# Kernel tuning notes

Measured on AMD Instinct MI355X. Metric: run time of the kernel, lower is better.

The kernel has to match this reference:

```python
import jax, jax.numpy as jnp
import numpy as np

N_INP = 1024
N_HID = 1024
N_OUT = 1024
B, S = 8, 2048


def setup_inputs() -> dict:
    key = jax.random.key(0)
    ks = jax.random.split(key, 9)
    s_in = 1.0 / np.sqrt(N_INP)
    s_hid = 1.0 / np.sqrt(N_HID)
    return {
        "x": jax.random.normal(ks[0], (B, S, N_INP), jnp.float32),
        "wq": jax.random.uniform(ks[1], (N_INP, N_HID), jnp.float32, -s_in, s_in),
        "bq": jax.random.uniform(ks[2], (N_HID,), jnp.float32, -s_in, s_in),
        "wk": jax.random.uniform(ks[3], (N_INP, N_HID), jnp.float32, -s_in, s_in),
        "bk": jax.random.uniform(ks[4], (N_HID,), jnp.float32, -s_in, s_in),
        "wv": jax.random.uniform(ks[5], (N_INP, N_HID), jnp.float32, -s_in, s_in),
        "bv": jax.random.uniform(ks[6], (N_HID,), jnp.float32, -s_in, s_in),
        "wo": jax.random.uniform(ks[7], (N_HID, N_OUT), jnp.float32, -s_hid, s_hid),
        "bo": jax.random.uniform(ks[8], (N_OUT,), jnp.float32, -s_hid, s_hid),
    }


def reference(x, wq, bq, wk, bk, wv, bv, wo, bo):
    # x: [B, S, n_inp]
    q = jnp.einsum("bsi,ih->bsh", x, wq) + bq  # [B,S,H]
    k = jnp.einsum("bsi,ih->bsh", x, wk) + bk
    v = jnp.einsum("bsi,ih->bsh", x, wv) + bv
    scale = 1.0 / jnp.sqrt(jnp.float32(N_HID))
    energy = jnp.einsum("bqh,bkh->bqk", q, k) * scale  # [B,S,S]
    attn = jax.nn.softmax(energy, axis=-1)  # dropout=0.0 (eval)
    ctx = jnp.einsum("bqk,bkh->bqh", attn, v)  # [B,S,H]
    out = jnp.einsum("bsh,ho->bso", ctx, wo) + bo  # [B,S,n_out]
    return out
```

## Files before the change

kernel.cpp:

```cpp
#include <hip/hip_runtime.h>
#include <hip/hip_bf16.h>


typedef __attribute__((ext_vector_type(8))) __bf16 bf16x8;
typedef __attribute__((ext_vector_type(4))) __bf16 bf16x4;
typedef __attribute__((ext_vector_type(4))) float  f32x4;
typedef __attribute__((ext_vector_type(8))) float  f32x8;

__device__ __forceinline__ void gl_lds16(const void* g, void* l) {
    __builtin_amdgcn_global_load_lds(
        (__attribute__((address_space(1))) const void*)g,
        (__attribute__((address_space(3))) void*)l, 16, 0, 0);
}

__global__ __launch_bounds__(256) void k_convert(const float* __restrict__ in,
                                                 __bf16* __restrict__ out) {
    const int i = blockIdx.x * 256 + threadIdx.x;
    f32x8 a = *((const f32x8*)in + i);
    bf16x8 o;
#pragma unroll
    for (int j = 0; j < 8; ++j) o[j] = (__bf16)a[j];
    *((bf16x8*)out + i) = o;
}

__global__ __launch_bounds__(256) void k_transpose_w(
    const float* __restrict__ w0, const float* __restrict__ w1,
    const float* __restrict__ w2, const float* __restrict__ w3,
    __bf16* __restrict__ Wt) {
    const int z = blockIdx.z;
    const float* W = (z == 0) ? w0 : (z == 1) ? w1 : (z == 2) ? w2 : w3;
    __bf16* Wo = Wt + (long long)z * 1048576;
    __shared__ float t[64][65];
    const int tid = threadIdx.x;
    const int c4 = (tid & 15) * 4, r0 = tid >> 4;
    const int bx = blockIdx.x * 64, by = blockIdx.y * 64;
#pragma unroll
    for (int p = 0; p < 4; ++p) {
        const int r = r0 + p * 16;
        f32x4 v = *(const f32x4*)(W + (long long)(by + r) * 1024 + bx + c4);
#pragma unroll
        for (int j = 0; j < 4; ++j) t[r][c4 + j] = v[j];
    }
    __syncthreads();
#pragma unroll
    for (int p = 0; p < 4; ++p) {
        const int r = r0 + p * 16;
        bf16x4 o;
#pragma unroll
        for (int j = 0; j < 4; ++j) o[j] = (__bf16)t[c4 + j][r];
        *(bf16x4*)(Wo + (long long)(bx + r) * 1024 + by + c4) = o;
    }
}

__global__ __launch_bounds__(256) void k_bcat(const float* __restrict__ bq,
                                              const float* __restrict__ bk,
                                              const float* __restrict__ bv,
                                              float* __restrict__ bc) {
    const int i = blockIdx.x * 256 + threadIdx.x;
    const float* s = (i < 1024) ? bq : (i < 2048 ? bk : bv);
    bc[i] = s[i & 1023];
}

__global__ __launch_bounds__(256) void k_softmax(__bf16* __restrict__ E) {
    __bf16* p = E + (long long)blockIdx.x * 2048;
    const int tid = threadIdx.x, l = tid & 63, w = tid >> 6;
    bf16x8 vb = *((const bf16x8*)p + tid);
    float v[8];
#pragma unroll
    for (int i = 0; i < 8; ++i) v[i] = (float)vb[i];
    float m = v[0];
#pragma unroll
    for (int i = 1; i < 8; ++i) m = fmaxf(m, v[i]);
    for (int off = 32; off > 0; off >>= 1) m = fmaxf(m, __shfl_xor(m, off));
    __shared__ float redm[4], reds[4];
    if (l == 0) redm[w] = m;
    __syncthreads();
    m = fmaxf(fmaxf(redm[0], redm[1]), fmaxf(redm[2], redm[3]));
    float e[8], s = 0.f;
#pragma unroll
    for (int i = 0; i < 8; ++i) { e[i] = __expf(v[i] - m); s += e[i]; }
    for (int off = 32; off > 0; off >>= 1) s += __shfl_xor(s, off);
    if (l == 0) reds[w] = s;
    __syncthreads();
    s = reds[0] + reds[1] + reds[2] + reds[3];
    const float inv = 1.0f / s;
    bf16x8 o;
#pragma unroll
    for (int i = 0; i < 8; ++i) o[i] = (__bf16)(e[i] * inv);
    *((bf16x8*)p + tid) = o;
}

template <int MODE, bool HAS_BIAS>
__global__ __launch_bounds__(512, 2) void gemm_bt(
    const __bf16* __restrict__ A, const __bf16* __restrict__ Bt,
    const float* __restrict__ bias, void* __restrict__ Cout,
    int K, int lda, int ldb, int ldc, int gy, int rpx, int bnc,
    float scale, long long sA, long long sB, long long sC) {
    __shared__ __align__(16) __bf16 Abuf0[16384];
    __shared__ __align__(16) __bf16 Bbuf0[16384];
    __shared__ __align__(16) __bf16 Abuf1[16384];
    __shared__ __align__(16) __bf16 Bbuf1[16384];

    const int lid = blockIdx.x;
    const int xcd = lid & 7;
    const int jj = lid >> 3;
    const int bn = jj % bnc;
    const int rt = xcd * rpx + jj / bnc;
    const int z = rt / gy;
    const int bm = rt - z * gy;

    const __bf16* Ab = A + (long long)z * sA;
    const __bf16* Bb = Bt + (long long)z * sB;

    const int tid = threadIdx.x;
    const int l = tid & 63, w = tid >> 6;
    const int wm = w >> 2, wn = w & 3;

    const int rA = tid >> 3;
    const int cswz = (tid & 7) ^ (rA & 3);
    const __bf16* aSg = Ab + (long long)(bm * 256 + rA) * lda + cswz * 8;
    const __bf16* bSg = Bb + (long long)(bn * 256 + rA) * ldb + cswz * 8;
    const long long a64 = (long long)lda * 64;
    const long long b64 = (long long)ldb * 64;
    const int ldst = tid * 16;

    const int r16 = l & 15, kq4 = l >> 4;
    const int swz = kq4 ^ (r16 & 3);
    const int aro = (wm * 128 + r16) * 64 + swz * 8;
    const int bro = (wn * 64 + r16) * 64 + swz * 8;

    f32x4 acc[8][4] = {};
    bf16x8 bf[4][2];

#define ST_A(buf, j, t)                                                    \
    gl_lds16(aSg + (j) * a64 + (long long)(t) * 64,                        \
             (char*)(buf) + ldst + (j) * 8192)
#define ST_B(buf, j, t)                                                    \
    gl_lds16(bSg + (j) * b64 + (long long)(t) * 64,                        \
             (char*)(buf) + ldst + (j) * 8192)

#define RD_B(buf)                                                          \
    do {                                                                   \
        _Pragma("unroll") for (int ni = 0; ni < 4; ++ni) {                 \
            bf[ni][0] = *(const bf16x8*)((buf) + bro + ni * 1024);         \
            bf[ni][1] = *(const bf16x8*)((buf) + bro + ni * 1024 + 32);    \
        }                                                                  \
    } while (0)

#define WV4 asm volatile("s_waitcnt vmcnt(4)" ::: "memory")
#define WV0 asm volatile("s_waitcnt vmcnt(0)" ::: "memory")
#define NOW ((void)0)

#define PHASE(Abuf, p, RB, RBUF, STAGES, WAIT)                                 \
    do {                                                                      \
        bf16x8 af0k0 = *(const bf16x8*)((Abuf) + aro + (2 * (p)) * 1024);      \
        bf16x8 af0k1 = *(const bf16x8*)((Abuf) + aro + (2 * (p)) * 1024 + 32); \
        bf16x8 af1k0 = *(const bf16x8*)((Abuf) + aro + (2 * (p) + 1) * 1024);  \
        bf16x8 af1k1 = *(const bf16x8*)((Abuf) + aro + (2*(p)+1) * 1024 + 32); \
        if (RB) RD_B(RBUF);                                                   \
        STAGES;                                                               \
        __builtin_amdgcn_s_barrier();                                         \
        asm volatile("s_waitcnt lgkmcnt(0)" ::: "memory");                    \
        __builtin_amdgcn_sched_barrier(0);                                    \
        __builtin_amdgcn_s_setprio(1);                                        \
        _Pragma("unroll") for (int ni = 0; ni < 4; ++ni) {                    \
            acc[2 * (p)][ni] = __builtin_amdgcn_mfma_f32_16x16x32_bf16(       \
                af0k0, bf[ni][0], acc[2 * (p)][ni], 0, 0, 0);                 \
            acc[2 * (p)][ni] = __builtin_amdgcn_mfma_f32_16x16x32_bf16(       \
                af0k1, bf[ni][1], acc[2 * (p)][ni], 0, 0, 0);                 \
            acc[2 * (p) + 1][ni] = __builtin_amdgcn_mfma_f32_16x16x32_bf16(   \
                af1k0, bf[ni][0], acc[2 * (p) + 1][ni], 0, 0, 0);             \
            acc[2 * (p) + 1][ni] = __builtin_amdgcn_mfma_f32_16x16x32_bf16(   \
                af1k1, bf[ni][1], acc[2 * (p) + 1][ni], 0, 0, 0);             \
        }                                                                     \
        __builtin_amdgcn_s_setprio(0);                                        \
        WAIT;                                                                 \
        __builtin_amdgcn_sched_barrier(0);                                    \
        __builtin_amdgcn_s_barrier();                                         \
    } while (0)

    ST_B(Bbuf0, 0, 0); ST_B(Bbuf0, 1, 0); ST_B(Bbuf0, 2, 0); ST_B(Bbuf0, 3, 0);
    ST_A(Abuf0, 0, 0); ST_A(Abuf0, 1, 0); ST_A(Abuf0, 2, 0); ST_A(Abuf0, 3, 0);
    ST_B(Bbuf1, 0, 1); ST_B(Bbuf1, 1, 1); ST_B(Bbuf1, 2, 1); ST_B(Bbuf1, 3, 1);
    WV4;
    __builtin_amdgcn_s_barrier();

    const int NT = K >> 6;
    for (int t0 = 0; t0 + 3 < NT; t0 += 2) {
        PHASE(Abuf0, 0, 1, Bbuf0,
              (ST_A(Abuf1, 0, t0 + 1), ST_A(Abuf1, 1, t0 + 1),
               ST_A(Abuf1, 2, t0 + 1), ST_A(Abuf1, 3, t0 + 1)), NOW);
        PHASE(Abuf0, 1, 0, Bbuf0,
              (ST_B(Bbuf0, 0, t0 + 2), ST_B(Bbuf0, 1, t0 + 2)), NOW);
        PHASE(Abuf0, 2, 0, Bbuf0,
              (ST_B(Bbuf0, 2, t0 + 2), ST_B(Bbuf0, 3, t0 + 2)), NOW);
        PHASE(Abuf0, 3, 0, Bbuf0, NOW, WV4);
        PHASE(Abuf1, 0, 1, Bbuf1,
              (ST_A(Abuf0, 0, t0 + 2), ST_A(Abuf0, 1, t0 + 2)), NOW);
        PHASE(Abuf1, 1, 0, Bbuf1,
              (ST_A(Abuf0, 2, t0 + 2), ST_A(Abuf0, 3, t0 + 2)), NOW);
        PHASE(Abuf1, 2, 0, Bbuf1,
              (ST_B(Bbuf1, 0, t0 + 3), ST_B(Bbuf1, 1, t0 + 3)), NOW);
        PHASE(Abuf1, 3, 0, Bbuf1,
              (ST_B(Bbuf1, 2, t0 + 3), ST_B(Bbuf1, 3, t0 + 3)), WV4);
    }
    {
        PHASE(Abuf0, 0, 1, Bbuf0,
              (ST_A(Abuf1, 0, NT - 1), ST_A(Abuf1, 1, NT - 1),
               ST_A(Abuf1, 2, NT - 1), ST_A(Abuf1, 3, NT - 1)), NOW);
        PHASE(Abuf0, 1, 0, Bbuf0, NOW, NOW);
        PHASE(Abuf0, 2, 0, Bbuf0, NOW, NOW);
        PHASE(Abuf0, 3, 0, Bbuf0, NOW, WV0);
        PHASE(Abuf1, 0, 1, Bbuf1, NOW, NOW);
        PHASE(Abuf1, 1, 0, Bbuf1, NOW, NOW);
        PHASE(Abuf1, 2, 0, Bbuf1, NOW, NOW);
        PHASE(Abuf1, 3, 0, Bbuf1, NOW, NOW);
    }
#undef ST_A
#undef ST_B
#undef RD_B
#undef WV4
#undef WV0
#undef NOW
#undef PHASE

    const int quad = kq4;
    if (MODE == 2) {
        __bf16* Qb = (__bf16*)Cout;
        const int part = bn >> 2;
#pragma unroll
        for (int mi = 0; mi < 8; ++mi) {
            const int srow0 = bm * 256 + wm * 128 + mi * 16 + quad * 4;
            const int b = srow0 >> 11;
            const int s0 = srow0 & 2047;
#pragma unroll
            for (int ni = 0; ni < 4; ++ni) {
                const int col = bn * 256 + wn * 64 + ni * 16 + r16;
                const float bb = HAS_BIAS ? bias[col] : 0.0f;
                const int c1 = col - part * 1024;
                if (part == 2) {
                    bf16x4 o;
#pragma unroll
                    for (int rr = 0; rr < 4; ++rr) o[rr] = (__bf16)(acc[mi][ni][rr] + bb);
                    *(bf16x4*)(Qb + 33554432 + (long long)b * 2097152 +
                               (long long)c1 * 2048 + s0) = o;
                } else {
                    __bf16* dst = Qb + (long long)part * 16777216 +
                                  (long long)b * 2097152 + (long long)s0 * 1024 + c1;
#pragma unroll
                    for (int rr = 0; rr < 4; ++rr) dst[rr * 1024] = (__bf16)(acc[mi][ni][rr] + bb);
                }
            }
        }
    } else {
        const long long cbase = (long long)z * sC;
#pragma unroll
        for (int mi = 0; mi < 8; ++mi) {
#pragma unroll
            for (int ni = 0; ni < 4; ++ni) {
                const int col = bn * 256 + wn * 64 + ni * 16 + r16;
                const float bb = HAS_BIAS ? bias[col] : 0.0f;
#pragma unroll
                for (int rr = 0; rr < 4; ++rr) {
                    const int row = bm * 256 + wm * 128 + mi * 16 + quad * 4 + rr;
                    const float v = acc[mi][ni][rr] * scale + bb;
                    if (MODE == 1)
                        ((float*)Cout)[cbase + (long long)row * ldc + col] = v;
                    else
                        ((__bf16*)Cout)[cbase + (long long)row * ldc + col] = (__bf16)v;
                }
            }
        }
    }
}

extern "C" void kernel_launch(void* const* d_in, const int* in_sizes, int n_in,
                              void* d_out, int out_size, void* d_ws, size_t ws_size,
                              hipStream_t stream) {
    const float* x  = (const float*)d_in[0];
    const float* wq = (const float*)d_in[1];
    const float* bq = (const float*)d_in[2];
    const float* wk = (const float*)d_in[3];
    const float* bk = (const float*)d_in[4];
    const float* wv = (const float*)d_in[5];
    const float* bv = (const float*)d_in[6];
    const float* wo = (const float*)d_in[7];
    const float* bo = (const float*)d_in[8];
    float* out = (float*)d_out;

    __bf16* ws  = (__bf16*)d_ws;
    __bf16* Xb  = ws;
    __bf16* E   = ws;
    __bf16* Q   = ws + 33554432;
    __bf16* Kb  = ws + 50331648;
    __bf16* Vt  = ws + 67108864;
    __bf16* Ctx = ws + 83886080;
    __bf16* WT  = ws + 100663296;
    float*  bc  = (float*)(ws + 104857600);

    k_convert<<<8192, 256, 0, stream>>>(x, Xb);
    k_transpose_w<<<dim3(16, 16, 4), 256, 0, stream>>>(wq, wk, wv, wo, WT);
    k_bcat<<<12, 256, 0, stream>>>(bq, bk, bv, bc);

    gemm_bt<2, true><<<768, 512, 0, stream>>>(
        Xb, WT, bc, Q, 1024, 1024, 1024, 0, 64, 8, 12, 1.0f, 0, 0, 0);

    gemm_bt<0, false><<<512, 512, 0, stream>>>(
        Q, Kb, nullptr, E, 1024, 1024, 1024, 2048, 8, 8, 8,
        0.03125f, 2097152, 2097152, 4194304);

    k_softmax<<<16384, 256, 0, stream>>>(E);

    gemm_bt<0, false><<<256, 512, 0, stream>>>(
        E, Vt, nullptr, Ctx, 2048, 2048, 2048, 1024, 8, 8, 4,
        1.0f, 4194304, 2097152, 2097152);

    gemm_bt<1, true><<<256, 512, 0, stream>>>(
        Ctx, WT + 3145728, bo, out, 1024, 1024, 1024, 1024, 64, 8, 4,
        1.0f, 0, 0, 0);
}
```

Measured before the change: 456.6 us.

## Swap MFMA operands for row-vectorized epilogue stores and widen LDS swizzle

Swaps the A/B operands of the MFMA so each lane holds four consecutive output columns, which lets the epilogues for Q/K, the energy and context GEMMs and the final output write vectorized bf16x4/f32x4 stores with vector bias loads instead of scattered scalar stores. The transposed V projection is split into its own launch (MODE 4) that keeps the original operand order, so its transposed layout still gets contiguous stores. The LDS XOR swizzle widens from 4 to 8 chunks to cut bank conflicts on fragment reads. The cost is one extra kernel launch and a smaller grid for the fused Q/K projection.

Result: faster. 446.8 us (-2.2%).

```diff
diff --git a/kernel.cpp b/kernel.cpp
--- a/kernel.cpp
+++ b/kernel.cpp
@@ -11,6 +11,14 @@
     __builtin_amdgcn_global_load_lds(
         (__attribute__((address_space(1))) const void*)g,
         (__attribute__((address_space(3))) void*)l, 16, 0, 0);
+}
+
+template <bool SWP>
+__device__ __forceinline__ f32x4 mfma16(bf16x8 a, bf16x8 b, f32x4 c) {
+    if constexpr (SWP)
+        return __builtin_amdgcn_mfma_f32_16x16x32_bf16(b, a, c, 0, 0, 0);
+    else
+        return __builtin_amdgcn_mfma_f32_16x16x32_bf16(a, b, c, 0, 0, 0);
 }
 
 __global__ __launch_bounds__(256) void k_convert(const float* __restrict__ in,
@@ -96,6 +104,7 @@
     const float* __restrict__ bias, void* __restrict__ Cout,
     int K, int lda, int ldb, int ldc, int gy, int rpx, int bnc,
     float scale, long long sA, long long sB, long long sC) {
+    constexpr bool SWP = (MODE != 4);
     __shared__ __align__(16) __bf16 Abuf0[16384];
     __shared__ __align__(16) __bf16 Bbuf0[16384];
     __shared__ __align__(16) __bf16 Abuf1[16384];
@@ -117,7 +126,7 @@
     const int wm = w >> 2, wn = w & 3;
 
     const int rA = tid >> 3;
-    const int cswz = (tid & 7) ^ (rA & 3);
+    const int cswz = (tid & 7) ^ (rA & 7);
     const __bf16* aSg = Ab + (long long)(bm * 256 + rA) * lda + cswz * 8;
     const __bf16* bSg = Bb + (long long)(bn * 256 + rA) * ldb + cswz * 8;
     const long long a64 = (long long)lda * 64;
@@ -125,9 +134,11 @@
     const int ldst = tid * 16;
 
     const int r16 = l & 15, kq4 = l >> 4;
-    const int swz = kq4 ^ (r16 & 3);
-    const int aro = (wm * 128 + r16) * 64 + swz * 8;
-    const int bro = (wn * 64 + r16) * 64 + swz * 8;
+    const int sw0 = kq4 ^ (r16 & 7);
+    const int aro0 = (wm * 128 + r16) * 64 + sw0 * 8;
+    const int aro1 = aro0 ^ 32;
+    const int bro0 = (wn * 64 + r16) * 64 + sw0 * 8;
+    const int bro1 = bro0 ^ 32;
 
     f32x4 acc[8][4] = {};
     bf16x8 bf[4][2];
@@ -142,8 +153,8 @@
 #define RD_B(buf)                                                          \
     do {                                                                   \
         _Pragma("unroll") for (int ni = 0; ni < 4; ++ni) {                 \
-            bf[ni][0] = *(const bf16x8*)((buf) + bro + ni * 1024);         \
-            bf[ni][1] = *(const bf16x8*)((buf) + bro + ni * 1024 + 32);    \
+            bf[ni][0] = *(const bf16x8*)((buf) + bro0 + ni * 1024);        \
+            bf[ni][1] = *(const bf16x8*)((buf) + bro1 + ni * 1024);        \
         }                                                                  \
     } while (0)
 
@@ -153,10 +164,10 @@
 
 #define PHASE(Abuf, p, RB, RBUF, STAGES, WAIT)                                 \
     do {                                                                      \
-        bf16x8 af0k0 = *(const bf16x8*)((Abuf) + aro + (2 * (p)) * 1024);      \
-        bf16x8 af0k1 = *(const bf16x8*)((Abuf) + aro + (2 * (p)) * 1024 + 32); \
-        bf16x8 af1k0 = *(const bf16x8*)((Abuf) + aro + (2 * (p) + 1) * 1024);  \
-        bf16x8 af1k1 = *(const bf16x8*)((Abuf) + aro + (2*(p)+1) * 1024 + 32); \
+        bf16x8 af0k0 = *(const bf16x8*)((Abuf) + aro0 + (2 * (p)) * 1024);     \
+        bf16x8 af0k1 = *(const bf16x8*)((Abuf) + aro1 + (2 * (p)) * 1024);     \
+        bf16x8 af1k0 = *(const bf16x8*)((Abuf) + aro0 + (2 * (p) + 1) * 1024); \
+        bf16x8 af1k1 = *(const bf16x8*)((Abuf) + aro1 + (2 * (p) + 1) * 1024); \
         if (RB) RD_B(RBUF);                                                   \
         STAGES;                                                               \
         __builtin_amdgcn_s_barrier();                                         \
@@ -164,14 +175,10 @@
         __builtin_amdgcn_sched_barrier(0);                                    \
         __builtin_amdgcn_s_setprio(1);                                        \
         _Pragma("unroll") for (int ni = 0; ni < 4; ++ni) {                    \
-            acc[2 * (p)][ni] = __builtin_amdgcn_mfma_f32_16x16x32_bf16(       \
-                af0k0, bf[ni][0], acc[2 * (p)][ni], 0, 0, 0);                 \
-            acc[2 * (p)][ni] = __builtin_amdgcn_mfma_f32_16x16x32_bf16(       \
-                af0k1, bf[ni][1], acc[2 * (p)][ni], 0, 0, 0);                 \
-            acc[2 * (p) + 1][ni] = __builtin_amdgcn_mfma_f32_16x16x32_bf16(   \
-                af1k0, bf[ni][0], acc[2 * (p) + 1][ni], 0, 0, 0);             \
-            acc[2 * (p) + 1][ni] = __builtin_amdgcn_mfma_f32_16x16x32_bf16(   \
-                af1k1, bf[ni][1], acc[2 * (p) + 1][ni], 0, 0, 0);             \
+            acc[2 * (p)][ni] = mfma16<SWP>(af0k0, bf[ni][0], acc[2*(p)][ni]); \
+            acc[2 * (p)][ni] = mfma16<SWP>(af0k1, bf[ni][1], acc[2*(p)][ni]); \
+            acc[2*(p)+1][ni] = mfma16<SWP>(af1k0, bf[ni][0], acc[2*(p)+1][ni]);\
+            acc[2*(p)+1][ni] = mfma16<SWP>(af1k1, bf[ni][1], acc[2*(p)+1][ni]);\
         }                                                                     \
         __builtin_amdgcn_s_setprio(0);                                        \
         WAIT;                                                                 \
@@ -225,9 +232,28 @@
 #undef PHASE
 
     const int quad = kq4;
-    if (MODE == 2) {
+    if constexpr (MODE == 2) {
         __bf16* Qb = (__bf16*)Cout;
         const int part = bn >> 2;
+#pragma unroll
+        for (int mi = 0; mi < 8; ++mi) {
+            const int srow0 = bm * 256 + wm * 128 + mi * 16 + r16;
+            const int b = srow0 >> 11;
+            const int s0 = srow0 & 2047;
+#pragma unroll
+            for (int ni = 0; ni < 4; ++ni) {
+                const int col0 = bn * 256 + wn * 64 + ni * 16 + quad * 4;
+                const f32x4 bb = *(const f32x4*)(bias + col0);
+                const int c1 = col0 - part * 1024;
+                bf16x4 o;
+#pragma unroll
+                for (int rr = 0; rr < 4; ++rr) o[rr] = (__bf16)(acc[mi][ni][rr] + bb[rr]);
+                *(bf16x4*)(Qb + (long long)part * 16777216 +
+                           (long long)b * 2097152 + (long long)s0 * 1024 + c1) = o;
+            }
+        }
+    } else if constexpr (MODE == 4) {
+        __bf16* Vb = (__bf16*)Cout;
 #pragma unroll
         for (int mi = 0; mi < 8; ++mi) {
             const int srow0 = bm * 256 + wm * 128 + mi * 16 + quad * 4;
@@ -235,39 +261,39 @@
             const int s0 = srow0 & 2047;
 #pragma unroll
             for (int ni = 0; ni < 4; ++ni) {
-                const int col = bn * 256 + wn * 64 + ni * 16 + r16;
-                const float bb = HAS_BIAS ? bias[col] : 0.0f;
-                const int c1 = col - part * 1024;
-                if (part == 2) {
-                    bf16x4 o;
-#pragma unroll
-                    for (int rr = 0; rr < 4; ++rr) o[rr] = (__bf16)(acc[mi][ni][rr] + bb);
-                    *(bf16x4*)(Qb + 33554432 + (long long)b * 2097152 +
-                               (long long)c1 * 2048 + s0) = o;
-                } else {
-                    __bf16* dst = Qb + (long long)part * 16777216 +
-                                  (long long)b * 2097152 + (long long)s0 * 1024 + c1;
-#pragma unroll
-                    for (int rr = 0; rr < 4; ++rr) dst[rr * 1024] = (__bf16)(acc[mi][ni][rr] + bb);
-                }
+                const int c1 = bn * 256 + wn * 64 + ni * 16 + r16;
+                const float bb = HAS_BIAS ? bias[c1] : 0.0f;
+                bf16x4 o;
+#pragma unroll
+                for (int rr = 0; rr < 4; ++rr) o[rr] = (__bf16)(acc[mi][ni][rr] + bb);
+                *(bf16x4*)(Vb + (long long)b * 2097152 +
+                           (long long)c1 * 2048 + s0) = o;
             }
         }
     } else {
         const long long cbase = (long long)z * sC;
 #pragma unroll
         for (int mi = 0; mi < 8; ++mi) {
+            const int row = bm * 256 + wm * 128 + mi * 16 + r16;
 #pragma unroll
             for (int ni = 0; ni < 4; ++ni) {
-                const int col = bn * 256 + wn * 64 + ni * 16 + r16;
-                const float bb = HAS_BIAS ? bias[col] : 0.0f;
-#pragma unroll
-                for (int rr = 0; rr < 4; ++rr) {
-                    const int row = bm * 256 + wm * 128 + mi * 16 + quad * 4 + rr;
-                    const float v = acc[mi][ni][rr] * scale + bb;
-                    if (MODE == 1)
-                        ((float*)Cout)[cbase + (long long)row * ldc + col] = v;
-                    else
-                        ((__bf16*)Cout)[cbase + (long long)row * ldc + col] = (__bf16)v;
+                const int col0 = bn * 256 + wn * 64 + ni * 16 + quad * 4;
+                f32x4 v;
+                if constexpr (HAS_BIAS) {
+                    const f32x4 bb = *(const f32x4*)(bias + col0);
+#pragma unroll
+                    for (int rr = 0; rr < 4; ++rr) v[rr] = acc[mi][ni][rr] * scale + bb[rr];
+                } else {
+#pragma unroll
+                    for (int rr = 0; rr < 4; ++rr) v[rr] = acc[mi][ni][rr] * scale;
+                }
+                if constexpr (MODE == 1) {
+                    *(f32x4*)((float*)Cout + cbase + (long long)row * ldc + col0) = v;
+                } else {
+                    bf16x4 o;
+#pragma unroll
+                    for (int rr = 0; rr < 4; ++rr) o[rr] = (__bf16)v[rr];
+                    *(bf16x4*)((__bf16*)Cout + cbase + (long long)row * ldc + col0) = o;
                 }
             }
         }
@@ -302,8 +328,12 @@
     k_transpose_w<<<dim3(16, 16, 4), 256, 0, stream>>>(wq, wk, wv, wo, WT);
     k_bcat<<<12, 256, 0, stream>>>(bq, bk, bv, bc);
 
-    gemm_bt<2, true><<<768, 512, 0, stream>>>(
-        Xb, WT, bc, Q, 1024, 1024, 1024, 0, 64, 8, 12, 1.0f, 0, 0, 0);
+    gemm_bt<2, true><<<512, 512, 0, stream>>>(
+        Xb, WT, bc, Q, 1024, 1024, 1024, 0, 64, 8, 8, 1.0f, 0, 0, 0);
+
+    gemm_bt<4, true><<<256, 512, 0, stream>>>(
+        Xb, WT + 2097152, bc + 2048, Vt, 1024, 1024, 1024, 0, 64, 8, 4,
+        1.0f, 0, 0, 0);
 
     gemm_bt<0, false><<<512, 512, 0, stream>>>(
         Q, Kb, nullptr, E, 1024, 1024, 1024, 2048, 8, 8, 8,
```
